# Kernel optimization log

Hardware: AMD Instinct MI355X
Metric: run time of the kernel (lower is better)

The kernel has to match this reference:

```python
import jax, jax.numpy as jnp
import numpy as np

N = 384      # max_nodes
H = 256      # layers[0] == layers[1] == layers[2]
Z = 128      # dim_z
ED = 128     # edge_dim
AH = ED // 2 # attention hidden

# complete directed graph: combinations (i<j) then reversed pairs
_i, _j = np.triu_indices(N, k=1)
_SRC = jnp.asarray(np.concatenate([_i, _j]), dtype=jnp.int32)  # edge_index[0]
_DST = jnp.asarray(np.concatenate([_j, _i]), dtype=jnp.int32)  # edge_index[1]


def setup_inputs() -> dict:
    key = jax.random.key(0)
    ks = jax.random.split(key, 16)
    def p(k, shape, fan_in):
        return jax.random.normal(k, shape, dtype=jnp.float32) * (1.0 / np.sqrt(fan_in))
    return {
        "z": jax.random.normal(ks[0], (1, Z), dtype=jnp.float32),
        # GRU (torch layout: W_ih [3H, Z], W_hh [3H, H]; gate order r, z, n)
        "gru_Wih": p(ks[1], (3 * H, Z), Z),
        "gru_Whh": p(ks[2], (3 * H, H), H),
        "gru_bih": jnp.zeros((3 * H,), jnp.float32),
        "gru_bhh": jnp.zeros((3 * H,), jnp.float32),
        # edge_generator MLP: 2H -> 4H -> ED
        "eg_W1": p(ks[3], (2 * H, 4 * H), 2 * H), "eg_b1": jnp.zeros((4 * H,), jnp.float32),
        "eg_W2": p(ks[4], (4 * H, ED), 4 * H),   "eg_b2": jnp.zeros((ED,), jnp.float32),
        # attention MLPs: (ED+H) -> ED//2 -> 1
        "att0_W1": p(ks[5], (ED + H, AH), ED + H), "att0_b1": jnp.zeros((AH,), jnp.float32),
        "att0_W2": p(ks[6], (AH, 1), AH),           "att0_b2": jnp.zeros((1,), jnp.float32),
        "att1_W1": p(ks[7], (ED + H, AH), ED + H), "att1_b1": jnp.zeros((AH,), jnp.float32),
        "att1_W2": p(ks[8], (AH, 1), AH),           "att1_b2": jnp.zeros((1,), jnp.float32),
        # EdgeConv output linears: H -> H
        "conv0_W": p(ks[9], (H, H), H),  "conv0_b": jnp.zeros((H,), jnp.float32),
        "conv1_W": p(ks[10], (H, H), H), "conv1_b": jnp.zeros((H,), jnp.float32),
    }


def _forward(z, gru_Wih, gru_Whh, gru_bih, gru_bhh,
             eg_W1, eg_b1, eg_W2, eg_b2,
             att0_W1, att0_b1, att0_W2, att0_b2,
             att1_W1, att1_b1, att1_W2, att1_b2,
             conv0_W, conv0_b, conv1_W, conv1_b):
    # --- GRU node generation: input is the same latent z at every step ---
    gi = z[0] @ gru_Wih.T + gru_bih            # [3H], constant per step
    gir, giz, gin = jnp.split(gi, 3)
    def step(h, _):
        gh = h @ gru_Whh.T + gru_bhh
        ghr, ghz, ghn = jnp.split(gh, 3)
        r = jax.nn.sigmoid(gir + ghr)
        u = jax.nn.sigmoid(giz + ghz)
        n = jnp.tanh(gin + r * ghn)
        h2 = (1.0 - u) * n + u * h
        return h2, h2
    _, nodes = jax.lax.scan(step, jnp.zeros((H,), z.dtype), None, length=N)  # [N, H]

    # --- edge features over the complete directed graph ---
    pairs = jnp.concatenate([nodes[_SRC], nodes[_DST]], axis=-1)            # [E, 2H]
    edges = jax.nn.relu(pairs @ eg_W1 + eg_b1) @ eg_W2 + eg_b2              # [E, ED]

    # --- EdgeConv: gather src, attention MLP gate, scatter-sum, linear ---
    def conv(x, aW1, ab1, aW2, ab2, W, b):
        xs = x[_SRC]                                                        # [E, H]
        a_in = jnp.concatenate([edges, xs], axis=-1)                        # [E, ED+H]
        att = jax.nn.sigmoid(jax.nn.relu(a_in @ aW1 + ab1) @ aW2 + ab2)     # [E, 1]
        agg = jax.ops.segment_sum(att * xs, _DST, num_segments=N)           # [N, H]
        return agg @ W + b

    x = jax.nn.relu(conv(nodes, att0_W1, att0_b1, att0_W2, att0_b2, conv0_W, conv0_b))
    x = conv(x, att1_W1, att1_b1, att1_W2, att1_b2, conv1_W, conv1_b)
    return jnp.sum(x, axis=0)                                               # [H]


def reference(z, gru_Wih, gru_Whh, gru_bih, gru_bhh,
              eg_W1, eg_b1, eg_W2, eg_b2,
              att0_W1, att0_b1, att0_W2, att0_b2,
              att1_W1, att1_b1, att1_W2, att1_b2,
              conv0_W, conv0_b, conv1_W, conv1_b):
    return _forward(z, gru_Wih, gru_Whh, gru_bih, gru_bhh,
                    eg_W1, eg_b1, eg_W2, eg_b2,
                    att0_W1, att0_b1, att0_W2, att0_b2,
                    att1_W1, att1_b1, att1_W2, att1_b2,
                    conv0_W, conv0_b, conv1_W, conv1_b)
```

## Files before the change

kernel.cpp:

```cpp
#include <hip/hip_runtime.h>
#include <hip/hip_fp16.h>
#include <cstdint>

#define DEV static __device__ __forceinline__

typedef _Float16 h2v __attribute__((ext_vector_type(2)));
typedef _Float16 half8 __attribute__((ext_vector_type(8)));
typedef float float4v __attribute__((ext_vector_type(4)));

union U32H2 { uint32_t u; _Float16 f[2]; };

DEV uint32_t pack_f2(float a, float b) {
    auto p = __builtin_amdgcn_cvt_pkrtz(a, b);
    return __builtin_bit_cast(uint32_t, p);
}

DEV half8 bc8(uint4 v) { return __builtin_bit_cast(half8, v); }

DEV void gl_lds16(const void* gsrc, void* ldst) {
    __builtin_amdgcn_global_load_lds(
        (const __attribute__((address_space(1))) uint32_t*)gsrc,
        (__attribute__((address_space(3))) uint32_t*)ldst, 16, 0, 0);
}

DEV float pick4(float4v lo, float4v hi, int bsel, int r) {
    float v0 = bsel ? hi[0] : lo[0];
    float v1 = bsel ? hi[1] : lo[1];
    float v2 = bsel ? hi[2] : lo[2];
    float v3 = bsel ? hi[3] : lo[3];
    float x01 = (r & 1) ? v1 : v0;
    float x23 = (r & 1) ? v3 : v2;
    return (r & 2) ? x23 : x01;
}

static const size_t OFF_W16T  = 0;
static const size_t OFF_GI    = 98304;
static const size_t OFF_CC    = 99072;
static const size_t OFF_BF    = 99200;
static const size_t OFF_NODES = 164736;
static const size_t OFF_PF    = 263040;
static const size_t OFF_QF    = 459648;
static const size_t OFF_R0    = 656256;
static const size_t OFF_R1    = 680832;
static const size_t OFF_TT    = 705408;
static const size_t OFF_ATT0  = 10142592;
static const size_t OFF_ATT1  = 10290048;
static const size_t OFF_X0    = 10535808;
static const size_t OFF_CS    = 10634112;
static const size_t WS_TOTAL  = 10634816;

__global__ void k_prep_wl(const float* __restrict__ Whh, uint32_t* __restrict__ WL,
                          const float* __restrict__ z, const float* __restrict__ Wih,
                          const float* __restrict__ bih, const float* __restrict__ bhh,
                          float* __restrict__ gs) {
    int bb = blockIdx.x, tid = threadIdx.x;
    if (bb < 48) {
        int c = bb;
        int rt = c >> 3, kt = c & 7;
        int lane = tid & 63, wv = tid >> 6;
        int row = (rt >> 1) * 256 + wv * 32 + ((rt & 1) << 4) + (lane & 15);
        int k0 = kt*32 + (lane >> 4)*8;
        const float* src = Whh + row*256 + k0;
        uint4 o;
        o.x = pack_f2(src[0], src[1]);
        o.y = pack_f2(src[2], src[3]);
        o.z = pack_f2(src[4], src[5]);
        o.w = pack_f2(src[6], src[7]);
        ((uint4*)WL)[c*512 + tid] = o;
    } else {
        int o = (bb - 48) * 512 + tid;
        if (o < 768) {
            float acc = bih[o];
            if (o < 512) acc += bhh[o];
            for (int i = 0; i < 128; ++i) acc += Wih[o*128 + i] * z[i];
            gs[o] = acc;
        }
    }
}

DEV void gru_run(const float* __restrict__ gs, const float* __restrict__ bhh,
                 const uint32_t* __restrict__ WL, float* __restrict__ nodes,
                 _Float16* hh16, int tid, int t0, int t1) {
    int lane = tid & 63, wv = tid >> 6;
    int kq = lane >> 4, c = lane & 15;
    const float L2E = 1.44269504088896f;
    int r = c & 3, bsel = (c >> 2) & 1;
    int gidx = wv*32 + kq*4 + r + bsel*16;
    bool active = (c < 8);

    uint4 w[48];
    const uint4* wl4 = (const uint4*)WL;
    #pragma unroll
    for (int q = 0; q < 48; ++q) w[q] = wl4[q*512 + tid];
    #pragma unroll
    for (int q = 0; q < 48; ++q)
        asm volatile("" : "+a"(w[q].x), "+a"(w[q].y), "+a"(w[q].z), "+a"(w[q].w));

    float pr = -L2E * gs[gidx];
    float pz = -L2E * gs[256 + gidx];
    float pn = -2.f * L2E * gs[512 + gidx];
    float bn_l = bhh[512 + gidx];

    float h;
    if (t0 == 0) {
        h = 0.f;
        if (tid < 256) ((uint32_t*)hh16)[tid] = 0u;
    } else {
        h = nodes[(size_t)(t0-1)*256 + gidx];
        if (tid < 256) hh16[tid] = (_Float16)nodes[(size_t)(t0-1)*256 + tid];
    }
    __syncthreads();

    const float4v z4 = {0.f, 0.f, 0.f, 0.f};
    int par = 0;
    for (int t = t0; t < t1; ++t) {
        const _Float16* hb = hh16 + par*256 + kq*8;
        uint4 b[8];
        #pragma unroll
        for (int kt = 0; kt < 8; ++kt) b[kt] = *(const uint4*)(hb + kt*32);

        float4v d0, d1, d2, d3, d4, d5;
        d0 = __builtin_amdgcn_mfma_f32_16x16x32_f16(bc8(w[0]),  bc8(b[0]), z4, 0, 0, 0);
        d1 = __builtin_amdgcn_mfma_f32_16x16x32_f16(bc8(w[8]),  bc8(b[0]), z4, 0, 0, 0);
        #pragma unroll
        for (int kt = 1; kt < 8; ++kt) {
            d0 = __builtin_amdgcn_mfma_f32_16x16x32_f16(bc8(w[kt]),   bc8(b[kt]), d0, 0, 0, 0);
            d1 = __builtin_amdgcn_mfma_f32_16x16x32_f16(bc8(w[8+kt]), bc8(b[kt]), d1, 0, 0, 0);
        }
        float ghr = pick4(d0, d1, bsel, r);
        float er = __builtin_amdgcn_exp2f(__builtin_fmaf(ghr, -L2E, pr));
        float rg = __builtin_amdgcn_rcpf(1.f + er);

        d2 = __builtin_amdgcn_mfma_f32_16x16x32_f16(bc8(w[16]), bc8(b[0]), z4, 0, 0, 0);
        d3 = __builtin_amdgcn_mfma_f32_16x16x32_f16(bc8(w[24]), bc8(b[0]), z4, 0, 0, 0);
        d4 = __builtin_amdgcn_mfma_f32_16x16x32_f16(bc8(w[32]), bc8(b[0]), z4, 0, 0, 0);
        d5 = __builtin_amdgcn_mfma_f32_16x16x32_f16(bc8(w[40]), bc8(b[0]), z4, 0, 0, 0);
        #pragma unroll
        for (int kt = 1; kt < 8; ++kt) {
            d2 = __builtin_amdgcn_mfma_f32_16x16x32_f16(bc8(w[16+kt]), bc8(b[kt]), d2, 0, 0, 0);
            d3 = __builtin_amdgcn_mfma_f32_16x16x32_f16(bc8(w[24+kt]), bc8(b[kt]), d3, 0, 0, 0);
            d4 = __builtin_amdgcn_mfma_f32_16x16x32_f16(bc8(w[32+kt]), bc8(b[kt]), d4, 0, 0, 0);
            d5 = __builtin_amdgcn_mfma_f32_16x16x32_f16(bc8(w[40+kt]), bc8(b[kt]), d5, 0, 0, 0);
        }

        float ghz = pick4(d2, d3, bsel, r);
        float ghn = pick4(d4, d5, bsel, r);
        float eu = __builtin_amdgcn_exp2f(__builtin_fmaf(ghz, -L2E, pz));
        float u  = __builtin_amdgcn_rcpf(1.f + eu);
        float tm = ghn + bn_l;
        float q  = __builtin_fmaf(rg * tm, -2.f * L2E, pn);
        float e2 = __builtin_amdgcn_exp2f(q);
        float nn = __builtin_fmaf(2.f, __builtin_amdgcn_rcpf(1.f + e2), -1.f);
        h = nn + u * (h - nn);

        if (active) {
            hh16[(par ^ 1)*256 + gidx] = (_Float16)h;
            nodes[(size_t)t*256 + gidx] = h;
        }
        asm volatile("s_waitcnt lgkmcnt(0)" ::: "memory");
        __builtin_amdgcn_sched_barrier(0);
        __builtin_amdgcn_s_barrier();
        __builtin_amdgcn_sched_barrier(0);
        par ^= 1;
    }
}

DEV void pq8_body(const float* __restrict__ nodes, const float* __restrict__ egW1,
                  const float* __restrict__ egb1, const float* __restrict__ a0W1,
                  const float* __restrict__ a0b1, const float* __restrict__ cc,
                  uint32_t* __restrict__ PF, uint32_t* __restrict__ QF,
                  float* __restrict__ R0, int s0, int tid, float* ns) {
    for (int i = tid; i < 2048; i += 512)
        ns[i] = nodes[(size_t)s0*256 + i];
    __syncthreads();

    int tp = tid & 255;
    int k0 = tp * 4;
    bool isQ = tid >= 256;
    float acc[8][4];
    #pragma unroll
    for (int q = 0; q < 8; ++q) { acc[q][0]=0;acc[q][1]=0;acc[q][2]=0;acc[q][3]=0; }
    const float* Wbase = egW1 + (isQ ? (size_t)256*1024 : 0) + k0;
    for (int i = 0; i < 256; ++i) {
        float4 wv = *(const float4*)&Wbase[(size_t)i*1024];
        #pragma unroll
        for (int q = 0; q < 8; ++q) {
            float nv = ns[q*256 + i];
            acc[q][0] += nv*wv.x; acc[q][1] += nv*wv.y;
            acc[q][2] += nv*wv.z; acc[q][3] += nv*wv.w;
        }
    }
    if (!isQ) {
        float4 bv = *(const float4*)&egb1[k0];
        int kk = k0 >> 5;
        int lgrp = ((k0 >> 3) & 3) * 16;
        int sub = (k0 & 7) >> 1;
        #pragma unroll
        for (int q = 0; q < 8; ++q) {
            int s = s0 + q, g = s >> 4, srow = s & 15;
            uint2 pw;
            pw.x = pack_f2(acc[q][0] + bv.x, acc[q][1] + bv.y);
            pw.y = pack_f2(acc[q][2] + bv.z, acc[q][3] + bv.w);
            *(uint2*)(PF + (((g*32 + kk)*64 + lgrp + srow) << 2) + sub) = pw;
        }
    } else {
        #pragma unroll
        for (int q = 0; q < 8; ++q) {
            uint2 pw;
            pw.x = pack_f2(acc[q][0], acc[q][1]);
            pw.y = pack_f2(acc[q][2], acc[q][3]);
            ((uint2*)QF)[(size_t)(s0+q)*256 + tp] = pw;
        }
    }
    {
        int srow = tid >> 6, j = tid & 63;
        float racc = a0b1[j] + cc[j];
        for (int i = 0; i < 256; ++i) racc += ns[srow*256 + i] * a0W1[(128+i)*64 + j];
        R0[(size_t)(s0+srow)*64 + j] = racc;
    }
}

__global__ void __launch_bounds__(512, 2)
k_gruA_bf(const float* __restrict__ gs, const float* __restrict__ bhh,
          const uint32_t* __restrict__ WL, float* __restrict__ nodes,
          const float* __restrict__ egW2, const float* __restrict__ egb2,
          const float* __restrict__ a0W1, const float* __restrict__ a1W1,
          uint32_t* __restrict__ BF, float* __restrict__ cc) {
    int bb = blockIdx.x, tid = threadIdx.x;
    if (bb == 0) {
        __shared__ __align__(16) _Float16 hh16[512];
        gru_run(gs, bhh, WL, nodes, hh16, tid, 0, 288);
    } else if (bb < 129) {
        int idx = (bb - 1) * 512 + tid;
        int k2 = idx >> 7, n = idx & 127;
        const float* A = (n < 64) ? (a0W1 + n) : (a1W1 + (n - 64));
        const float* w0 = egW2 + (2*k2) * 128;
        float a = 0.f, b = 0.f;
        for (int i = 0; i < 128; ++i) {
            float av = A[i*64];
            a += w0[i] * av;
            b += w0[128 + i] * av;
        }
        int kk = k2 >> 4, jgrp = (k2 >> 2) & 3, sub = k2 & 3;
        int lane = jgrp*16 + (n & 15), t = n >> 4;
        BF[((kk*8 + t)*64 + lane)*4 + sub] = pack_f2(a, b);
    } else {
        if (tid < 128) {
            const float* A = (tid < 64) ? a0W1 : a1W1;
            int j = tid & 63;
            float acc = 0.f;
            for (int i = 0; i < 128; ++i) acc += egb2[i] * A[i*64 + j];
            cc[tid] = acc;
        }
    }
}

__global__ void __launch_bounds__(512, 2)
k_gruB_pq(const float* __restrict__ gs, const float* __restrict__ bhh,
          const uint32_t* __restrict__ WL, float* __restrict__ nodes,
          const float* __restrict__ egW1, const float* __restrict__ egb1,
          const float* __restrict__ a0W1, const float* __restrict__ a0b1,
          const float* __restrict__ cc,
          uint32_t* __restrict__ PF, uint32_t* __restrict__ QF,
          float* __restrict__ R0) {
    __shared__ __align__(16) float smem_f[2048];
    int bb = blockIdx.x, tid = threadIdx.x;
    if (bb == 0) {
        gru_run(gs, bhh, WL, nodes, (_Float16*)smem_f, tid, 288, 384);
    } else {
        pq8_body(nodes, egW1, egb1, a0W1, a0b1, cc, PF, QF, R0, (bb - 1) * 8, tid, smem_f);
    }
}

__global__ void __launch_bounds__(512)
k_pq_tail(const float* __restrict__ nodes, const float* __restrict__ egW1,
          const float* __restrict__ egb1, const float* __restrict__ a0W1,
          const float* __restrict__ a0b1, const float* __restrict__ cc,
          uint32_t* __restrict__ PF, uint32_t* __restrict__ QF,
          float* __restrict__ R0) {
    __shared__ __align__(16) float smem_f[2048];
    pq8_body(nodes, egW1, egb1, a0W1, a0b1, cc, PF, QF, R0, 288 + blockIdx.x * 8,
             threadIdx.x, smem_f);
}

__global__ void __launch_bounds__(512, 4)
k_phaseA(const uint32_t* __restrict__ PF, const uint32_t* __restrict__ QF,
         const uint32_t* __restrict__ BF, const float* __restrict__ R0,
         const float* __restrict__ a0W2, const float* __restrict__ a0b2,
         uint32_t* __restrict__ TT, float* __restrict__ ATT0) {
    __shared__ __align__(16) char smem[69632];
    uint4* Qs4 = (uint4*)smem;
    char* bufbase = smem + 32768;
    int tid = threadIdx.x;
    int lane = tid & 63, wv = tid >> 6;
    int g = blockIdx.x, dt = blockIdx.y, d0 = dt * 16;

    {
        const char* src = (const char*)(QF + (size_t)d0 * 512);
        for (int off = tid*16; off < 32768; off += 8192)
            gl_lds16(src + off, (char*)Qs4 + off);
    }
    {
        const char* psrc = (const char*)(PF + (size_t)g * 8192);
        if (tid < 128) gl_lds16(psrc + tid*16, bufbase + tid*16);
        const char* bsrc = (const char*)BF;
        #pragma unroll
        for (int i = 0; i < 2; ++i)
            gl_lds16(bsrc + tid*16 + i*8192, bufbase + 2048 + tid*16 + i*8192);
    }
    asm volatile("s_waitcnt vmcnt(0)" ::: "memory");
    __builtin_amdgcn_sched_barrier(0);
    __builtin_amdgcn_s_barrier();
    __builtin_amdgcn_sched_barrier(0);

    float4v acc[2][8];
    #pragma unroll
    for (int t = 0; t < 2; ++t)
        #pragma unroll
        for (int n = 0; n < 8; ++n) acc[t][n] = 0.f;

    for (int hc = 0; hc < 16; ++hc) {
        char* cur = bufbase + (hc & 1) * 18432;
        char* nxt = bufbase + ((hc + 1) & 1) * 18432;
        if (hc < 15) {
            const char* psrc = (const char*)(PF + ((size_t)g*32 + (size_t)(hc+1)*2) * 256);
            if (tid < 128) gl_lds16(psrc + tid*16, nxt + tid*16);
            const char* bsrc = (const char*)(BF + (size_t)(hc+1) * 4096);
            #pragma unroll
            for (int i = 0; i < 2; ++i)
                gl_lds16(bsrc + tid*16 + i*8192, nxt + 2048 + tid*16 + i*8192);
        }
        uint4* Ph = (uint4*)cur;
        uint4* Bh = (uint4*)(cur + 2048);
        #pragma unroll
        for (int kkl = 0; kkl < 2; ++kkl) {
            int kkg = hc*2 + kkl;
            half8 b[8];
            #pragma unroll
            for (int n = 0; n < 8; ++n) b[n] = bc8(Bh[(kkl*8 + n)*64 + lane]);
            half8 p8 = bc8(Ph[kkl*64 + lane]);
            #pragma unroll
            for (int t = 0; t < 2; ++t) {
                half8 q8 = bc8(Qs4[(wv*2 + t)*128 + kkg*4 + (lane >> 4)]);
                half8 x = p8 + q8;
                half8 zz = 0;
                x = __builtin_elementwise_max(x, zz);
                #pragma unroll
                for (int n = 0; n < 8; ++n)
                    acc[t][n] = __builtin_amdgcn_mfma_f32_16x16x32_f16(x, b[n], acc[t][n], 0, 0, 0);
            }
        }
        asm volatile("s_waitcnt vmcnt(0)" ::: "memory");
        __builtin_amdgcn_sched_barrier(0);
        __builtin_amdgcn_s_barrier();
        __builtin_amdgcn_sched_barrier(0);
    }

    __syncthreads();
    float* R0s = (float*)smem;
    float* w2s = (float*)(smem + 4096);
    for (int i = tid; i < 1024; i += 512)
        R0s[i] = R0[(size_t)(g*16 + (i >> 6))*64 + (i & 63)];
    if (tid < 64) w2s[tid] = a0W2[tid];
    float b2v = a0b2[0];

    _Float16* epi = (_Float16*)(smem + 32768);
    int cn = lane & 15, rhi = (lane >> 4) * 4;
    for (int half = 0; half < 2; ++half) {
        __syncthreads();
        #pragma unroll
        for (int t = 0; t < 2; ++t) {
            int dl = wv*2 + t;
            #pragma unroll
            for (int n = 0; n < 4; ++n) {
                int j = n*16 + cn;
                float4v v = acc[t][half*4 + n];
                #pragma unroll
                for (int r = 0; r < 4; ++r)
                    epi[((rhi + r)*16 + dl)*64 + j] = (_Float16)v[r];
            }
        }
        __syncthreads();
        if (half == 1) {
            int p = tid >> 1, sub = tid & 1;
            int srow = p >> 4, dl = p & 15;
            const uint4* src = (const uint4*)(epi + (size_t)p*64);
            uint4* dst = (uint4*)(TT + ((size_t)((g*16 + srow)*384 + d0 + dl))*32);
            #pragma unroll
            for (int q = 0; q < 4; ++q) dst[sub*4 + q] = src[sub*4 + q];
        }
        if (half == 0 && tid < 256) {
            int sl = tid >> 4, dl = tid & 15;
            const _Float16* tp = epi + (size_t)(sl*16 + dl)*64;
            const float* rp = R0s + sl*64;
            float logit = b2v;
            #pragma unroll
            for (int j = 0; j < 64; ++j)
                logit += fmaxf((float)tp[j] + rp[j], 0.f) * w2s[j];
            float a = 1.f / (1.f + __expf(-logit));
            int s = g*16 + sl, d = d0 + dl;
            ATT0[(size_t)s*384 + d] = (s == d) ? 0.f : a;
        }
    }
}

__global__ void k_att(const uint32_t* __restrict__ TT, const float* __restrict__ R,
                      const float* __restrict__ w2, const float* __restrict__ b2,
                      float* __restrict__ CS) {
    int tid = threadIdx.x;
    int p = blockIdx.x * 256 + tid;
    int s = p / 384, d = p - s * 384;
    int sa = (blockIdx.x * 256) / 384;
    __shared__ float w2s[64];
    __shared__ float rs[2][64];
    if (tid < 64) w2s[tid] = w2[tid];
    else if (tid < 128) rs[0][tid - 64] = R[sa*64 + (tid - 64)];
    else if (tid < 192) {
        int sb = sa + 1;
        rs[1][tid - 128] = (sb < 384) ? R[sb*64 + (tid - 128)] : 0.f;
    }
    __syncthreads();
    const uint4* tp = (const uint4*)(TT + (size_t)p*32);
    const float* rp = (s == sa) ? rs[0] : rs[1];
    float logit = b2[0];
    #pragma unroll
    for (int m = 0; m < 8; ++m) {
        uint4 tv = tp[m];
        uint32_t us[4] = {tv.x, tv.y, tv.z, tv.w};
        #pragma unroll
        for (int q = 0; q < 4; ++q) {
            U32H2 c; c.u = us[q];
            int j = m*8 + q*2;
            float h0 = fmaxf((float)c.f[0] + rp[j],   0.f);
            float h1 = fmaxf((float)c.f[1] + rp[j+1], 0.f);
            logit += h0*w2s[j] + h1*w2s[j+1];
        }
    }
    float a = 1.f / (1.f + __expf(-logit));
    float a_eff = (s == d) ? 0.f : a;

    float va = (s == sa) ? a_eff : 0.f;
    float vb = (s != sa) ? a_eff : 0.f;
    #pragma unroll
    for (int o = 32; o > 0; o >>= 1) {
        va += __shfl_down(va, o, 64);
        vb += __shfl_down(vb, o, 64);
    }
    if ((tid & 63) == 0) {
        atomicAdd(&CS[sa], va);
        int sb = sa + 1;
        if (sb < 384) atomicAdd(&CS[sb], vb);
    }
}

__global__ void __launch_bounds__(256)
k_aggx0(const float* __restrict__ ATT, const float* __restrict__ X,
        const float* __restrict__ W, const float* __restrict__ b,
        const float* __restrict__ a1W1, const float* __restrict__ a1b1,
        const float* __restrict__ cc,
        float* __restrict__ X0, float* __restrict__ R1, float* __restrict__ CS) {
    int d = blockIdx.x, tid = threadIdx.x;
    if (d == 0) {
        for (int s = tid; s < 384; s += 256) CS[s] = 0.f;
    }
    __shared__ float att_col[384];
    __shared__ float ag[256];
    __shared__ float xs[256];
    for (int s = tid; s < 384; s += 256) att_col[s] = ATT[(size_t)s*384 + d];
    __syncthreads();
    float acc = 0.f;
    #pragma unroll 4
    for (int s = 0; s < 384; ++s)
        acc += att_col[s] * X[(size_t)s*256 + tid];
    ag[tid] = acc;
    __syncthreads();
    float x0 = b[tid];
    for (int i = 0; i < 256; ++i) x0 += ag[i] * W[i*256 + tid];
    x0 = fmaxf(x0, 0.f);
    X0[(size_t)d*256 + tid] = x0;
    xs[tid] = x0;
    __syncthreads();
    if (tid < 64) {
        float r = a1b1[tid] + cc[64 + tid];
        for (int i = 0; i < 256; ++i) r += xs[i] * a1W1[(128+i)*64 + tid];
        R1[(size_t)d*64 + tid] = r;
    }
}

__global__ void k_vout(const float* __restrict__ CS, const float* __restrict__ X0,
                       const float* __restrict__ W, const float* __restrict__ b,
                       float* __restrict__ out) {
    int tid = threadIdx.x;
    __shared__ float cs[384];
    __shared__ float vs[256];
    for (int q = tid; q < 384; q += 256) cs[q] = CS[q];
    __syncthreads();
    float acc = 0.f;
    for (int s = 0; s < 384; s += 4) {
        acc += cs[s]*X0[s*256 + tid] + cs[s+1]*X0[(s+1)*256 + tid]
             + cs[s+2]*X0[(s+2)*256 + tid] + cs[s+3]*X0[(s+3)*256 + tid];
    }
    vs[tid] = acc;
    __syncthreads();
    float o = 384.f * b[tid];
    for (int i = 0; i < 256; ++i) o += vs[i] * W[i*256 + tid];
    out[tid] = o;
}

extern "C" void kernel_launch(void* const* d_in, const int* in_sizes, int n_in,
                              void* d_out, int out_size, void* d_ws, size_t ws_size,
                              hipStream_t stream) {
    if (ws_size < WS_TOTAL * sizeof(uint32_t)) return;

    const float* z    = (const float*)d_in[0];
    const float* Wih  = (const float*)d_in[1];
    const float* Whh  = (const float*)d_in[2];
    const float* bih  = (const float*)d_in[3];
    const float* bhh  = (const float*)d_in[4];
    const float* egW1 = (const float*)d_in[5];
    const float* egb1 = (const float*)d_in[6];
    const float* egW2 = (const float*)d_in[7];
    const float* egb2 = (const float*)d_in[8];
    const float* a0W1 = (const float*)d_in[9];
    const float* a0b1 = (const float*)d_in[10];
    const float* a0W2 = (const float*)d_in[11];
    const float* a0b2 = (const float*)d_in[12];
    const float* a1W1 = (const float*)d_in[13];
    const float* a1b1 = (const float*)d_in[14];
    const float* a1W2 = (const float*)d_in[15];
    const float* a1b2 = (const float*)d_in[16];
    const float* c0W  = (const float*)d_in[17];
    const float* c0b  = (const float*)d_in[18];
    const float* c1W  = (const float*)d_in[19];
    const float* c1b  = (const float*)d_in[20];

    uint32_t* ws   = (uint32_t*)d_ws;
    uint32_t* WL   = ws + OFF_W16T;
    float*    gs   = (float*)(ws + OFF_GI);
    float*    cc   = (float*)(ws + OFF_CC);
    uint32_t* BF   = ws + OFF_BF;
    float*    nodes= (float*)(ws + OFF_NODES);
    uint32_t* PF   = ws + OFF_PF;
    uint32_t* QF   = ws + OFF_QF;
    float*    R0   = (float*)(ws + OFF_R0);
    float*    R1   = (float*)(ws + OFF_R1);
    uint32_t* TT   = ws + OFF_TT;
    float*    ATT0 = (float*)(ws + OFF_ATT0);
    float*    X0   = (float*)(ws + OFF_X0);
    float*    CS   = (float*)(ws + OFF_CS);
    float*    out  = (float*)d_out;

    hipLaunchKernelGGL(k_prep_wl, dim3(50),     dim3(512), 0, stream, Whh, WL, z, Wih, bih, bhh, gs);
    hipLaunchKernelGGL(k_gruA_bf, dim3(130),    dim3(512), 0, stream, gs, bhh, WL, nodes,
                       egW2, egb2, a0W1, a1W1, BF, cc);
    hipLaunchKernelGGL(k_gruB_pq, dim3(37),     dim3(512), 0, stream, gs, bhh, WL, nodes,
                       egW1, egb1, a0W1, a0b1, cc, PF, QF, R0);
    hipLaunchKernelGGL(k_pq_tail, dim3(12),     dim3(512), 0, stream, nodes, egW1, egb1,
                       a0W1, a0b1, cc, PF, QF, R0);
    hipLaunchKernelGGL(k_phaseA,  dim3(24, 24), dim3(512), 0, stream, PF, QF, BF, R0, a0W2, a0b2, TT, ATT0);
    hipLaunchKernelGGL(k_aggx0,   dim3(384),    dim3(256), 0, stream, ATT0, nodes, c0W, c0b, a1W1, a1b1, cc, X0, R1, CS);
    hipLaunchKernelGGL(k_att,     dim3(576),    dim3(256), 0, stream, TT, R1, a1W2, a1b2, CS);
    hipLaunchKernelGGL(k_vout,    dim3(1),      dim3(256), 0, stream, CS, X0, c1W, c1b, out);
}
```

Measured before the change: 650.4 us.

## Overlap PQ tail with phaseA tiles, fuse vout into k_att via last-block reduction

Splits phaseA into two launches. The first runs the tiles whose P/Q rows are already complete from the GRU stage, alongside the extra blocks that compute the remaining PQ tail. The second handles the tiles that depend on the tail rows. The final k_vout kernel is folded into k_att with an atomic completion counter, so the last block does the output projection, and the R1 matvec in k_aggx0 is split across four wave groups. This removes two launches and lets independent work overlap, but adds the counter reset and atomic ordering, and lowers the occupancy hint for phaseA from 4 to 2.

```diff
diff --git a/kernel.cpp b/kernel.cpp
--- a/kernel.cpp
+++ b/kernel.cpp
@@ -44,7 +44,7 @@
 static const size_t OFF_R1    = 680832;
 static const size_t OFF_TT    = 705408;
 static const size_t OFF_ATT0  = 10142592;
-static const size_t OFF_ATT1  = 10290048;
+static const size_t OFF_DONE  = 10290048;
 static const size_t OFF_X0    = 10535808;
 static const size_t OFF_CS    = 10634112;
 static const size_t WS_TOTAL  = 10634816;
@@ -272,28 +272,36 @@
     }
 }
 
-__global__ void __launch_bounds__(512)
-k_pq_tail(const float* __restrict__ nodes, const float* __restrict__ egW1,
-          const float* __restrict__ egb1, const float* __restrict__ a0W1,
-          const float* __restrict__ a0b1, const float* __restrict__ cc,
-          uint32_t* __restrict__ PF, uint32_t* __restrict__ QF,
-          float* __restrict__ R0) {
-    __shared__ __align__(16) float smem_f[2048];
-    pq8_body(nodes, egW1, egb1, a0W1, a0b1, cc, PF, QF, R0, 288 + blockIdx.x * 8,
-             threadIdx.x, smem_f);
-}
-
-__global__ void __launch_bounds__(512, 4)
+__global__ void __launch_bounds__(512, 2)
 k_phaseA(const uint32_t* __restrict__ PF, const uint32_t* __restrict__ QF,
          const uint32_t* __restrict__ BF, const float* __restrict__ R0,
          const float* __restrict__ a0W2, const float* __restrict__ a0b2,
-         uint32_t* __restrict__ TT, float* __restrict__ ATT0) {
+         uint32_t* __restrict__ TT, float* __restrict__ ATT0,
+         const float* __restrict__ nodes, const float* __restrict__ egW1,
+         const float* __restrict__ egb1, const float* __restrict__ a0W1,
+         const float* __restrict__ a0b1, const float* __restrict__ cc,
+         uint32_t* __restrict__ PFw, uint32_t* __restrict__ QFw,
+         float* __restrict__ R0w, int variant) {
     __shared__ __align__(16) char smem[69632];
+    int tid = threadIdx.x;
+    int g, dt;
+    if (variant == 1) {
+        if (blockIdx.x >= 324) {
+            pq8_body(nodes, egW1, egb1, a0W1, a0b1, cc, PFw, QFw, R0w,
+                     288 + (blockIdx.x - 324) * 8, tid, (float*)smem);
+            return;
+        }
+        g = blockIdx.x / 18; dt = blockIdx.x % 18;
+    } else {
+        int id = blockIdx.x;
+        if (id < 144) { dt = 18 + id / 24; g = id % 24; }
+        else { int id2 = id - 144; g = 18 + id2 / 18; dt = id2 % 18; }
+    }
+    int d0 = dt * 16;
+
     uint4* Qs4 = (uint4*)smem;
     char* bufbase = smem + 32768;
-    int tid = threadIdx.x;
     int lane = tid & 63, wv = tid >> 6;
-    int g = blockIdx.x, dt = blockIdx.y, d0 = dt * 16;
 
     {
         const char* src = (const char*)(QF + (size_t)d0 * 512);
@@ -406,7 +414,9 @@
 
 __global__ void k_att(const uint32_t* __restrict__ TT, const float* __restrict__ R,
                       const float* __restrict__ w2, const float* __restrict__ b2,
-                      float* __restrict__ CS) {
+                      float* __restrict__ CS, uint32_t* __restrict__ done,
+                      const float* __restrict__ X0, const float* __restrict__ c1W,
+                      const float* __restrict__ c1b, float* __restrict__ out) {
     int tid = threadIdx.x;
     int p = blockIdx.x * 256 + tid;
     int s = p / 384, d = p - s * 384;
@@ -451,6 +461,32 @@
         int sb = sa + 1;
         if (sb < 384) atomicAdd(&CS[sb], vb);
     }
+
+    __threadfence();
+    __syncthreads();
+    __shared__ int last_s;
+    if (tid == 0) {
+        uint32_t v = __hip_atomic_fetch_add(done, 1u, __ATOMIC_ACQ_REL, __HIP_MEMORY_SCOPE_AGENT);
+        last_s = (v == 575);
+    }
+    __syncthreads();
+    if (!last_s) return;
+
+    __shared__ float cs[384];
+    __shared__ float vs[256];
+    for (int q = tid; q < 384; q += 256)
+        cs[q] = __hip_atomic_load(&CS[q], __ATOMIC_ACQUIRE, __HIP_MEMORY_SCOPE_AGENT);
+    __syncthreads();
+    float acc = 0.f;
+    for (int ss = 0; ss < 384; ss += 4) {
+        acc += cs[ss]*X0[ss*256 + tid] + cs[ss+1]*X0[(ss+1)*256 + tid]
+             + cs[ss+2]*X0[(ss+2)*256 + tid] + cs[ss+3]*X0[(ss+3)*256 + tid];
+    }
+    vs[tid] = acc;
+    __syncthreads();
+    float o = 384.f * c1b[tid];
+    for (int i = 0; i < 256; ++i) o += vs[i] * c1W[i*256 + tid];
+    out[tid] = o;
 }
 
 __global__ void __launch_bounds__(256)
@@ -458,14 +494,17 @@
         const float* __restrict__ W, const float* __restrict__ b,
         const float* __restrict__ a1W1, const float* __restrict__ a1b1,
         const float* __restrict__ cc,
-        float* __restrict__ X0, float* __restrict__ R1, float* __restrict__ CS) {
+        float* __restrict__ X0, float* __restrict__ R1,
+        float* __restrict__ CS, uint32_t* __restrict__ done) {
     int d = blockIdx.x, tid = threadIdx.x;
     if (d == 0) {
         for (int s = tid; s < 384; s += 256) CS[s] = 0.f;
+        if (tid == 0) *done = 0u;
     }
     __shared__ float att_col[384];
     __shared__ float ag[256];
     __shared__ float xs[256];
+    __shared__ float part[4][64];
     for (int s = tid; s < 384; s += 256) att_col[s] = ATT[(size_t)s*384 + d];
     __syncthreads();
     float acc = 0.f;
@@ -480,31 +519,18 @@
     X0[(size_t)d*256 + tid] = x0;
     xs[tid] = x0;
     __syncthreads();
+    {
+        int j = tid & 63, qd = tid >> 6;
+        float r = 0.f;
+        int i0 = qd * 64;
+        for (int i = i0; i < i0 + 64; ++i) r += xs[i] * a1W1[(128+i)*64 + j];
+        part[qd][j] = r;
+    }
+    __syncthreads();
     if (tid < 64) {
-        float r = a1b1[tid] + cc[64 + tid];
-        for (int i = 0; i < 256; ++i) r += xs[i] * a1W1[(128+i)*64 + tid];
-        R1[(size_t)d*64 + tid] = r;
-    }
-}
-
-__global__ void k_vout(const float* __restrict__ CS, const float* __restrict__ X0,
-                       const float* __restrict__ W, const float* __restrict__ b,
-                       float* __restrict__ out) {
-    int tid = threadIdx.x;
-    __shared__ float cs[384];
-    __shared__ float vs[256];
-    for (int q = tid; q < 384; q += 256) cs[q] = CS[q];
-    __syncthreads();
-    float acc = 0.f;
-    for (int s = 0; s < 384; s += 4) {
-        acc += cs[s]*X0[s*256 + tid] + cs[s+1]*X0[(s+1)*256 + tid]
-             + cs[s+2]*X0[(s+2)*256 + tid] + cs[s+3]*X0[(s+3)*256 + tid];
-    }
-    vs[tid] = acc;
-    __syncthreads();
-    float o = 384.f * b[tid];
-    for (int i = 0; i < 256; ++i) o += vs[i] * W[i*256 + tid];
-    out[tid] = o;
+        R1[(size_t)d*64 + tid] = a1b1[tid] + cc[64 + tid]
+            + part[0][tid] + part[1][tid] + part[2][tid] + part[3][tid];
+    }
 }
 
 extern "C" void kernel_launch(void* const* d_in, const int* in_sizes, int n_in,
@@ -546,19 +572,22 @@
     float*    R1   = (float*)(ws + OFF_R1);
     uint32_t* TT   = ws + OFF_TT;
     float*    ATT0 = (float*)(ws + OFF_ATT0);
+    uint32_t* done = ws + OFF_DONE;
     float*    X0   = (float*)(ws + OFF_X0);
     float*    CS   = (float*)(ws + OFF_CS);
     float*    out  = (float*)d_out;
 
-    hipLaunchKernelGGL(k_prep_wl, dim3(50),     dim3(512), 0, stream, Whh, WL, z, Wih, bih, bhh, gs);
-    hipLaunchKernelGGL(k_gruA_bf, dim3(130),    dim3(512), 0, stream, gs, bhh, WL, nodes,
+    hipLaunchKernelGGL(k_prep_wl, dim3(50),  dim3(512), 0, stream, Whh, WL, z, Wih, bih, bhh, gs);
+    hipLaunchKernelGGL(k_gruA_bf, dim3(130), dim3(512), 0, stream, gs, bhh, WL, nodes,
                        egW2, egb2, a0W1, a1W1, BF, cc);
-    hipLaunchKernelGGL(k_gruB_pq, dim3(37),     dim3(512), 0, stream, gs, bhh, WL, nodes,
+    hipLaunchKernelGGL(k_gruB_pq, dim3(37),  dim3(512), 0, stream, gs, bhh, WL, nodes,
                        egW1, egb1, a0W1, a0b1, cc, PF, QF, R0);
-    hipLaunchKernelGGL(k_pq_tail, dim3(12),     dim3(512), 0, stream, nodes, egW1, egb1,
-                       a0W1, a0b1, cc, PF, QF, R0);
-    hipLaunchKernelGGL(k_phaseA,  dim3(24, 24), dim3(512), 0, stream, PF, QF, BF, R0, a0W2, a0b2, TT, ATT0);
-    hipLaunchKernelGGL(k_aggx0,   dim3(384),    dim3(256), 0, stream, ATT0, nodes, c0W, c0b, a1W1, a1b1, cc, X0, R1, CS);
-    hipLaunchKernelGGL(k_att,     dim3(576),    dim3(256), 0, stream, TT, R1, a1W2, a1b2, CS);
-    hipLaunchKernelGGL(k_vout,    dim3(1),      dim3(256), 0, stream, CS, X0, c1W, c1b, out);
-}
+    hipLaunchKernelGGL(k_phaseA,  dim3(336), dim3(512), 0, stream, PF, QF, BF, R0, a0W2, a0b2,
+                       TT, ATT0, nodes, egW1, egb1, a0W1, a0b1, cc, PF, QF, R0, 1);
+    hipLaunchKernelGGL(k_phaseA,  dim3(252), dim3(512), 0, stream, PF, QF, BF, R0, a0W2, a0b2,
+                       TT, ATT0, nodes, egW1, egb1, a0W1, a0b1, cc, PF, QF, R0, 2);
+    hipLaunchKernelGGL(k_aggx0,   dim3(384), dim3(256), 0, stream, ATT0, nodes, c0W, c0b,
+                       a1W1, a1b1, cc, X0, R1, CS, done);
+    hipLaunchKernelGGL(k_att,     dim3(576), dim3(256), 0, stream, TT, R1, a1W2, a1b2,
+                       CS, done, X0, c1W, c1b, out);
+}
```

Result: slower. 682.2 us (+4.9%).
